# Optimization experiments

Hardware: AMD Instinct MI355X
Metric: run time of the kernel (lower is better)

Reference implementation:

```python
import jax, jax.numpy as jnp
import numpy as np

TEMPERATURE = 11.313708498984761  # sqrt(128)
TOP_K = 16
EPS = 10e-8


def sparse_attention(attn_s, top_k):
    # attn_s: [N, T]; keep top_k entries per row, shift by k-th value, clamp, renormalize
    T = attn_s.shape[1]
    if T <= top_k:
        return attn_s
    delta = jax.lax.top_k(attn_s, top_k)[0][:, -1] + EPS  # [N]
    w = jnp.maximum(attn_s - delta[:, None], 0.0)
    return w / (jnp.sum(w, axis=1, keepdims=True) + EPS)


def setup_inputs() -> dict:
    key = jax.random.key(0)
    kq, kk, kv = jax.random.split(key, 3)
    q = jax.random.normal(kq, (8, 4096, 128), dtype=jnp.float32)
    k = jax.random.normal(kk, (8, 4096, 128), dtype=jnp.float32)
    v = jax.random.normal(kv, (8, 1, 128), dtype=jnp.float32)
    return {"q": q, "k": k, "v": v}


def reference(q, k, v):
    # scores: [b, lq, lk]
    scores = jnp.einsum('bqd,bkd->bqk', q, k) / TEMPERATURE
    # max over keys (keepdim) then exp -> [b, lq, 1]
    scores = jnp.exp(jnp.max(scores, axis=-1, keepdims=True))
    b, lq, _ = scores.shape
    # flag=True: softmax over the query dimension (permute(0,2,1) then softmax(-1))
    attn = jax.nn.softmax(scores[:, :, 0], axis=-1)  # [b, lq]
    # Sparse_attention top-k over query dim (flag=True reshape path)
    sp = sparse_attention(attn, TOP_K)  # [b, lq]
    attn3 = sp[:, :, None]  # [b, lq, 1] (dropout p=0.0 -> identity)
    out = jnp.einsum('bqk,bkd->bqd', attn3, v)  # [b, lq, dv]
    extra_loss = 0.0
    return out, attn3, extra_loss
```

## Files before the change

### kernel.cpp

```cpp
#include <hip/hip_runtime.h>
#include <math.h>

typedef __attribute__((ext_vector_type(8)))  short short8v;
typedef __attribute__((ext_vector_type(4)))  short short4v;
typedef __attribute__((ext_vector_type(16))) float f32x16;

#define NB     8
#define SEQ    4096
#define DIM    128
#define KSPLIT 4
#define NSPAN  (SEQ / KSPLIT)
#define BN     64
#define BM     256
#define TEMP_INV (1.0f / 11.313708498984761f)
#define EPSF   1e-7f
#define NEGINF -3.0e38f

__device__ __forceinline__ unsigned short f2bf(float x) {
    unsigned u = __float_as_uint(x);
    return (unsigned short)((u + 0x7FFFu + ((u >> 16) & 1u)) >> 16);
}
__device__ __forceinline__ float bf2f(unsigned short h) {
    return __uint_as_float(((unsigned)h) << 16);
}
__device__ __forceinline__ unsigned umaxu(unsigned a, unsigned b) { return a > b ? a : b; }

#define GL_LDS16(gsrc, ldst)                                                              \
    __builtin_amdgcn_global_load_lds((const __attribute__((address_space(1))) void*)(gsrc), \
                                     (__attribute__((address_space(3))) void*)(ldst), 16, 0, 0)

__global__ __launch_bounds__(256) void split_khi_kernel(
    const float* __restrict__ kp, unsigned short* __restrict__ kh)
{
    int t    = blockIdx.x * 256 + threadIdx.x;
    int row  = t >> 2;
    int part = t & 3;
    const float* src = kp + (size_t)row * DIM + part * 32;
    unsigned short* dst = kh + (size_t)row * DIM;
    int key = (row & 15) << 3;
    #pragma unroll
    for (int c = 0; c < 4; ++c) {
        int d = part * 32 + c * 8;
        float4 x0 = *(const float4*)(src + c * 8);
        float4 x1 = *(const float4*)(src + c * 8 + 4);
        short8v h;
        h[0] = (short)f2bf(x0.x); h[1] = (short)f2bf(x0.y);
        h[2] = (short)f2bf(x0.z); h[3] = (short)f2bf(x0.w);
        h[4] = (short)f2bf(x1.x); h[5] = (short)f2bf(x1.y);
        h[6] = (short)f2bf(x1.z); h[7] = (short)f2bf(x1.w);
        *(short8v*)(dst + (d ^ key)) = h;
    }
}

__global__ __launch_bounds__(512, 4) void max_hi_kernel(
    const float* __restrict__ qp, const unsigned short* __restrict__ khp,
    unsigned int* __restrict__ cand)
{
    __shared__ __align__(16) unsigned short kbuf[2][BN * DIM];

    const int bid   = blockIdx.x;
    const int batch = bid & 7;
    const int qt    = (bid >> 3) & 15;
    const int ks    = bid >> 7;

    const int tid   = threadIdx.x;
    const int wv    = tid >> 6;
    const int lane  = tid & 63;
    const int lhalf = lane >> 5;
    const int l31   = lane & 31;
    const int qrow0 = qt * BM + wv * 32;

    const char* ktile0 = (const char*)(khp + ((size_t)(batch * SEQ + ks * NSPAN)) * DIM);
    const int   woff   = wv * 2048;

    #pragma unroll
    for (int r = 0; r < 2; ++r) {
        int off = woff + r * 1024;
        GL_LDS16(ktile0 + off + lane * 16, (char*)&kbuf[0][0] + off);
    }

    short8v ah[8];
    {
        const float* qrow = qp + ((size_t)(batch * SEQ + qrow0 + l31)) * DIM + lhalf * 8;
        #pragma unroll
        for (int ch = 0; ch < 8; ++ch) {
            float4 x0 = *(const float4*)(qrow + ch * 16);
            float4 x1 = *(const float4*)(qrow + ch * 16 + 4);
            short8v h;
            h[0] = (short)f2bf(x0.x); h[1] = (short)f2bf(x0.y);
            h[2] = (short)f2bf(x0.z); h[3] = (short)f2bf(x0.w);
            h[4] = (short)f2bf(x1.x); h[5] = (short)f2bf(x1.y);
            h[6] = (short)f2bf(x1.z); h[7] = (short)f2bf(x1.w);
            ah[ch] = h;
        }
    }

    unsigned pk0[16], pk1[16];
    #pragma unroll
    for (int r = 0; r < 16; ++r) { pk0[r] = 0u; pk1[r] = 0u; }

    __syncthreads();

    int cur = 0;
    for (int it = 0; it < NSPAN / BN; ++it) {
        if (it < NSPAN / BN - 1) {
            const char* src = ktile0 + (size_t)(it + 1) * (BN * 256);
            #pragma unroll
            for (int r = 0; r < 2; ++r) {
                int off = woff + r * 1024;
                GL_LDS16(src + off + lane * 16, (char*)&kbuf[cur ^ 1][0] + off);
            }
        }
        __builtin_amdgcn_s_setprio(1);
        const unsigned itb = (unsigned)it;
        #pragma unroll
        for (int ns = 0; ns < 2; ++ns) {
            const int  brow = ns * 32 + l31;
            const int  bkey = (l31 & 15) << 3;
            const char* base = (const char*)&kbuf[cur][0] + brow * 256;
            f32x16 c;
            #pragma unroll
            for (int r = 0; r < 16; ++r) c[r] = 0.f;
            #pragma unroll
            for (int ch = 0; ch < 8; ++ch) {
                const int boff = 2 * ((ch * 16 + lhalf * 8) ^ bkey);
                short8v bh = *(const short8v*)(base + boff);
                c = __builtin_amdgcn_mfma_f32_32x32x16_bf16(ah[ch], bh, c, 0, 0, 0);
            }
            #pragma unroll
            for (int r = 0; r < 16; ++r) {
                unsigned pv = (__float_as_uint(c[r] + 128.f) & 0xFFFFFFF0u) | itb;
                if (ns == 0) pk0[r] = umaxu(pk0[r], pv);
                else         pk1[r] = umaxu(pk1[r], pv);
            }
        }
        __builtin_amdgcn_s_setprio(0);
        __syncthreads();
        cur ^= 1;
    }

    #pragma unroll
    for (int r = 0; r < 16; ++r) {
        unsigned k0 = pk0[r], k1v = pk1[r];
        unsigned i0  = ((k0 & 15u) << 6)  | l31;
        unsigned i1v = ((k1v & 15u) << 6) | 32u | l31;
        unsigned t1, t1i, t2, t2i;
        if (k0 >= k1v) { t1 = k0;  t1i = i0;  t2 = k1v; t2i = i1v; }
        else           { t1 = k1v; t1i = i1v; t2 = k0;  t2i = i0;  }
        #pragma unroll
        for (int off = 1; off <= 16; off <<= 1) {
            unsigned o1  = (unsigned)__shfl_xor((int)t1,  off, 64);
            unsigned o1i = (unsigned)__shfl_xor((int)t1i, off, 64);
            unsigned o2  = (unsigned)__shfl_xor((int)t2,  off, 64);
            unsigned o2i = (unsigned)__shfl_xor((int)t2i, off, 64);
            bool og = o1 > t1;
            unsigned n1  = og ? o1  : t1;
            unsigned n1i = og ? o1i : t1i;
            unsigned a2  = og ? t1  : o1;
            unsigned a2i = og ? t1i : o1i;
            unsigned b2  = og ? o2  : t2;
            unsigned b2i = og ? o2i : t2i;
            bool ag = a2 > b2;
            t1 = n1; t1i = n1i;
            t2 = ag ? a2 : b2; t2i = ag ? a2i : b2i;
        }
        if (l31 == 0) {
            int rr = (r & 3) + 8 * (r >> 2) + 4 * lhalf;
            cand[((size_t)(batch * SEQ + qrow0 + rr)) * KSPLIT + ks] =
                (t1i & 0xFFFFu) | (t2i << 16);
        }
    }
}

__global__ __launch_bounds__(256) void rescore_kernel(
    const float* __restrict__ qp, const float* __restrict__ kp,
    const unsigned int* __restrict__ cand, float* __restrict__ mq)
{
    const int row  = blockIdx.x * 4 + (threadIdx.x >> 6);
    const int lane = threadIdx.x & 63;
    const int b    = row >> 12;
    const int g    = lane >> 3;
    const int t8   = lane & 7;
    const int ks   = g >> 1;
    unsigned cc  = cand[(size_t)row * KSPLIT + ks];
    unsigned idx = (g & 1) ? (cc >> 16) : (cc & 0xFFFFu);
    const float* qrow = qp + (size_t)row * DIM + t8 * 16;
    const float* krow = kp + ((size_t)(b * SEQ + ks * NSPAN + (int)idx)) * DIM + t8 * 16;
    float s = 0.f;
    #pragma unroll
    for (int i = 0; i < 4; ++i) {
        float4 a  = *(const float4*)(qrow + i * 4);
        float4 kk = *(const float4*)(krow + i * 4);
        s += a.x * kk.x + a.y * kk.y + a.z * kk.z + a.w * kk.w;
    }
    #pragma unroll
    for (int off = 1; off <= 4; off <<= 1) s += __shfl_xor(s, off, 64);
    #pragma unroll
    for (int off = 8; off <= 32; off <<= 1) s = fmaxf(s, __shfl_xor(s, off, 64));
    if (lane == 0) mq[row] = s * TEMP_INV;
}

__global__ __launch_bounds__(512, 2) void max_scores_kernel(
    const float* __restrict__ qp, const float* __restrict__ kp,
    float* __restrict__ mpart)
{
    __shared__ short khi[BN * DIM];
    __shared__ short klo[BN * DIM];

    const int bid   = blockIdx.x;
    const int batch = bid & 7;
    const int qt    = (bid >> 3) & 15;
    const int ks    = bid >> 7;
    const int tid   = threadIdx.x;
    const int wv    = tid >> 6;
    const int lane  = tid & 63;
    const int lhalf = lane >> 5;
    const int l31   = lane & 31;
    const int qrow0 = qt * BM + wv * 32;

    short8v ah[8], al[8];
    {
        const float* qrow = qp + ((size_t)(batch * SEQ + qrow0 + l31)) * DIM + lhalf * 8;
        #pragma unroll
        for (int ch = 0; ch < 8; ++ch) {
            float4 x0 = *(const float4*)(qrow + ch * 16);
            float4 x1 = *(const float4*)(qrow + ch * 16 + 4);
            float xs[8] = {x0.x, x0.y, x0.z, x0.w, x1.x, x1.y, x1.z, x1.w};
            short8v h, l;
            #pragma unroll
            for (int j = 0; j < 8; ++j) {
                unsigned short hb = f2bf(xs[j]);
                h[j] = (short)hb;
                l[j] = (short)f2bf(xs[j] - bf2f(hb));
            }
            ah[ch] = h; al[ch] = l;
        }
    }

    f32x16 mx;
    #pragma unroll
    for (int r = 0; r < 16; ++r) mx[r] = NEGINF;

    const int srow = tid >> 3;
    const int soct = tid & 7;
    const int skey = (srow & 15) << 3;

    for (int it = 0; it < NSPAN / BN; ++it) {
        const int n0 = ks * NSPAN + it * BN;
        __syncthreads();
        {
            const float* ksrc = kp + ((size_t)(batch * SEQ + n0 + srow)) * DIM + soct * 16;
            #pragma unroll
            for (int i = 0; i < 4; ++i) {
                float4 x = *(const float4*)(ksrc + i * 4);
                int dq  = soct * 16 + i * 4;
                int idx = srow * DIM + (dq ^ skey);
                float xs[4] = {x.x, x.y, x.z, x.w};
                short4v h, l;
                #pragma unroll
                for (int j = 0; j < 4; ++j) {
                    unsigned short hb = f2bf(xs[j]);
                    h[j] = (short)hb;
                    l[j] = (short)f2bf(xs[j] - bf2f(hb));
                }
                *(short4v*)(&khi[idx]) = h;
                *(short4v*)(&klo[idx]) = l;
            }
        }
        __syncthreads();

        #pragma unroll
        for (int ns = 0; ns < 2; ++ns) {
            const int brow = ns * 32 + l31;
            const int bkey = (brow & 15) << 3;
            f32x16 c;
            #pragma unroll
            for (int r = 0; r < 16; ++r) c[r] = 0.f;
            #pragma unroll
            for (int ch = 0; ch < 8; ++ch) {
                const int d0  = ch * 16 + lhalf * 8;
                const int idx = brow * DIM + (d0 ^ bkey);
                short8v bh = *(const short8v*)(&khi[idx]);
                short8v bl = *(const short8v*)(&klo[idx]);
                c = __builtin_amdgcn_mfma_f32_32x32x16_bf16(ah[ch], bh, c, 0, 0, 0);
                c = __builtin_amdgcn_mfma_f32_32x32x16_bf16(al[ch], bh, c, 0, 0, 0);
                c = __builtin_amdgcn_mfma_f32_32x32x16_bf16(ah[ch], bl, c, 0, 0, 0);
            }
            #pragma unroll
            for (int r = 0; r < 16; ++r) mx[r] = fmaxf(mx[r], c[r]);
        }
    }

    #pragma unroll
    for (int r = 0; r < 16; ++r) {
        float v = mx[r];
        #pragma unroll
        for (int off = 16; off; off >>= 1)
            v = fmaxf(v, __shfl_xor(v, off, 64));
        mx[r] = v;
    }
    if (l31 == 0) {
        #pragma unroll
        for (int r = 0; r < 16; ++r) {
            int rr = (r & 3) + 8 * (r >> 2) + 4 * lhalf;
            mpart[((size_t)(batch * SEQ + qrow0 + rr)) * KSPLIT + ks] = mx[r] * TEMP_INV;
        }
    }
}

__global__ void reduce4_kernel(const float* __restrict__ mpart, float* __restrict__ mq)
{
    int i = blockIdx.x * 256 + threadIdx.x;
    float4 mp = *(const float4*)(mpart + (size_t)i * 4);
    mq[i] = fmaxf(fmaxf(mp.x, mp.y), fmaxf(mp.z, mp.w));
}

__global__ __launch_bounds__(1024) void softmax_topk2_kernel(
    const float* __restrict__ mq, float* __restrict__ attn_out,
    float* __restrict__ loss_out)
{
    const int b    = blockIdx.x;
    const int tid  = threadIdx.x;
    const int wv   = tid >> 6;
    const int lane = tid & 63;
    __shared__ float cand[256];
    __shared__ float smZ[16], smW[16];
    __shared__ float bc[2];

    float m[4];
    #pragma unroll
    for (int j = 0; j < 4; ++j) m[j] = mq[b * SEQ + tid + j * 1024];

    {
        float a0 = m[0], a1 = m[1], a2 = m[2], a3 = m[3];
        for (int pass = 0; pass < 16; ++pass) {
            float v = fmaxf(fmaxf(a0, a1), fmaxf(a2, a3));
            #pragma unroll
            for (int off = 32; off; off >>= 1) v = fmaxf(v, __shfl_xor(v, off, 64));
            bool has = (a0 == v) || (a1 == v) || (a2 == v) || (a3 == v);
            unsigned long long msk = __ballot(has);
            int leader = __ffsll(msk) - 1;
            if (lane == leader) {
                if (a0 == v) a0 = NEGINF;
                else if (a1 == v) a1 = NEGINF;
                else if (a2 == v) a2 = NEGINF;
                else a3 = NEGINF;
            }
            if (lane == pass) cand[wv * 16 + pass] = v;
        }
    }
    __syncthreads();

    if (wv == 0) {
        float a0 = cand[lane * 4 + 0], a1 = cand[lane * 4 + 1];
        float a2 = cand[lane * 4 + 2], a3 = cand[lane * 4 + 3];
        float first = 0.f, last = 0.f;
        for (int pass = 0; pass < 16; ++pass) {
            float v = fmaxf(fmaxf(a0, a1), fmaxf(a2, a3));
            #pragma unroll
            for (int off = 32; off; off >>= 1) v = fmaxf(v, __shfl_xor(v, off, 64));
            bool has = (a0 == v) || (a1 == v) || (a2 == v) || (a3 == v);
            unsigned long long msk = __ballot(has);
            int leader = __ffsll(msk) - 1;
            if (lane == leader) {
                if (a0 == v) a0 = NEGINF;
                else if (a1 == v) a1 = NEGINF;
                else if (a2 == v) a2 = NEGINF;
                else a3 = NEGINF;
            }
            if (pass == 0) first = v;
            last = v;
        }
        if (lane == 0) { bc[0] = first; bc[1] = last; }
    }
    __syncthreads();

    const float S   = expf(bc[0]);
    const float m16 = bc[1];

    float e[4]; float ls = 0.f;
    #pragma unroll
    for (int j = 0; j < 4; ++j) { e[j] = expf(expf(m[j]) - S); ls += e[j]; }
    #pragma unroll
    for (int off = 32; off; off >>= 1) ls += __shfl_xor(ls, off, 64);
    if (lane == 0) smZ[wv] = ls;
    __syncthreads();
    float Z = 0.f;
    #pragma unroll
    for (int i = 0; i < 16; ++i) Z += smZ[i];

    const float a16   = expf(expf(m16) - S) / Z;
    const float delta = a16 + EPSF;

    float w0[4]; float lw = 0.f;
    #pragma unroll
    for (int j = 0; j < 4; ++j) { w0[j] = fmaxf(e[j] / Z - delta, 0.f); lw += w0[j]; }
    #pragma unroll
    for (int off = 32; off; off >>= 1) lw += __shfl_xor(lw, off, 64);
    if (lane == 0) smW[wv] = lw;
    __syncthreads();
    float W = 0.f;
    #pragma unroll
    for (int i = 0; i < 16; ++i) W += smW[i];
    const float rW = 1.f / (W + EPSF);

    #pragma unroll
    for (int j = 0; j < 4; ++j)
        attn_out[b * SEQ + tid + j * 1024] = w0[j] * rW;
    if (b == 0 && tid == 0) loss_out[0] = 0.f;
}

__global__ void broadcast_out_kernel(const float* __restrict__ sp,
                                     const float* __restrict__ vp,
                                     float* __restrict__ outp)
{
    int gid = blockIdx.x * 256 + threadIdx.x;
    int row = gid >> 5;
    int c4  = gid & 31;
    float  s  = sp[row];
    float4 vv = *(const float4*)(vp + (row >> 12) * DIM + c4 * 4);
    float4 o; o.x = s * vv.x; o.y = s * vv.y; o.z = s * vv.z; o.w = s * vv.w;
    *(float4*)(outp + (size_t)gid * 4) = o;
}

extern "C" void kernel_launch(void* const* d_in, const int* in_sizes, int n_in,
                              void* d_out, int out_size, void* d_ws, size_t ws_size,
                              hipStream_t stream)
{
    (void)in_sizes; (void)n_in; (void)out_size;
    const float* q = (const float*)d_in[0];
    const float* k = (const float*)d_in[1];
    const float* v = (const float*)d_in[2];
    float* out  = (float*)d_out;
    float* attn = out + (size_t)NB * SEQ * DIM;
    float* loss = attn + (size_t)NB * SEQ;

    const size_t KH_BYTES   = (size_t)NB * SEQ * DIM * 2;
    const size_t CAND_BYTES = (size_t)NB * SEQ * KSPLIT * 4;
    const size_t MQ_BYTES   = (size_t)NB * SEQ * 4;

    if (ws_size >= KH_BYTES + CAND_BYTES + MQ_BYTES) {
        unsigned short* kh  = (unsigned short*)d_ws;
        unsigned int* cand  = (unsigned int*)((char*)d_ws + KH_BYTES);
        float* mq           = (float*)((char*)d_ws + KH_BYTES + CAND_BYTES);
        hipLaunchKernelGGL(split_khi_kernel, dim3(NB * SEQ * 4 / 256), dim3(256), 0, stream, k, kh);
        hipLaunchKernelGGL(max_hi_kernel, dim3(NB * (SEQ / BM) * KSPLIT), dim3(512), 0, stream,
                           q, kh, cand);
        hipLaunchKernelGGL(rescore_kernel, dim3(NB * SEQ / 4), dim3(256), 0, stream,
                           q, k, cand, mq);
        hipLaunchKernelGGL(softmax_topk2_kernel, dim3(NB), dim3(1024), 0, stream, mq, attn, loss);
    } else {
        float* mpart = (float*)d_ws;
        float* mq    = mpart + (size_t)NB * SEQ * KSPLIT;
        hipLaunchKernelGGL(max_scores_kernel, dim3(NB * (SEQ / BM) * KSPLIT), dim3(512), 0, stream,
                           q, k, mpart);
        hipLaunchKernelGGL(reduce4_kernel, dim3(NB * SEQ / 256), dim3(256), 0, stream, mpart, mq);
        hipLaunchKernelGGL(softmax_topk2_kernel, dim3(NB), dim3(1024), 0, stream, mq, attn, loss);
    }
    hipLaunchKernelGGL(broadcast_out_kernel, dim3((NB * SEQ * DIM / 4) / 256), dim3(256), 0, stream,
                       attn, v, out);
}
```

Baseline: 166.3 us.

## Enlarge max-score tiles so each wave computes two query blocks per K fragment

The bf16 max-score kernel now uses 512-row query tiles and 128-key K tiles. Each wave holds two 32-row query fragments and reuses every LDS K fragment for two MFMA chains, which halves LDS reads per MFMA and halves the grid. The +128 bias is folded into the initial accumulator, and the packed key/index now uses a 5-bit field. The candidate tracking changes from top-2 per lane over two column blocks to top-1 per lane, then a top-2 shuffle reduction. The cost is higher register pressure (occupancy hint lowered to 2), double the LDS per block, and fewer mantissa bits kept in the packed max.

```diff
diff --git a/kernel.cpp b/kernel.cpp
--- a/kernel.cpp
+++ b/kernel.cpp
@@ -12,6 +12,9 @@
 #define NSPAN  (SEQ / KSPLIT)
 #define BN     64
 #define BM     256
+#define BN2    128
+#define BM2    512
+#define ITERS  (NSPAN / BN2)
 #define TEMP_INV (1.0f / 11.313708498984761f)
 #define EPSF   1e-7f
 #define NEGINF -3.0e38f
@@ -52,36 +55,37 @@
     }
 }
 
-__global__ __launch_bounds__(512, 4) void max_hi_kernel(
+__global__ __launch_bounds__(512, 2) void max_hi2_kernel(
     const float* __restrict__ qp, const unsigned short* __restrict__ khp,
     unsigned int* __restrict__ cand)
 {
-    __shared__ __align__(16) unsigned short kbuf[2][BN * DIM];
+    __shared__ __align__(16) unsigned short kbuf[2][BN2 * DIM];
 
     const int bid   = blockIdx.x;
     const int batch = bid & 7;
-    const int qt    = (bid >> 3) & 15;
-    const int ks    = bid >> 7;
+    const int qt    = (bid >> 3) & 7;
+    const int ks    = bid >> 6;
 
     const int tid   = threadIdx.x;
     const int wv    = tid >> 6;
     const int lane  = tid & 63;
     const int lhalf = lane >> 5;
     const int l31   = lane & 31;
-    const int qrow0 = qt * BM + wv * 32;
+    const int qrow0 = qt * BM2 + wv * 64;
 
     const char* ktile0 = (const char*)(khp + ((size_t)(batch * SEQ + ks * NSPAN)) * DIM);
-    const int   woff   = wv * 2048;
-
-    #pragma unroll
-    for (int r = 0; r < 2; ++r) {
+    const int   woff   = wv * 4096;
+
+    #pragma unroll
+    for (int r = 0; r < 4; ++r) {
         int off = woff + r * 1024;
         GL_LDS16(ktile0 + off + lane * 16, (char*)&kbuf[0][0] + off);
     }
 
-    short8v ah[8];
-    {
-        const float* qrow = qp + ((size_t)(batch * SEQ + qrow0 + l31)) * DIM + lhalf * 8;
+    short8v ah[2][8];
+    #pragma unroll
+    for (int s = 0; s < 2; ++s) {
+        const float* qrow = qp + ((size_t)(batch * SEQ + qrow0 + s * 32 + l31)) * DIM + lhalf * 8;
         #pragma unroll
         for (int ch = 0; ch < 8; ++ch) {
             float4 x0 = *(const float4*)(qrow + ch * 16);
@@ -91,9 +95,13 @@
             h[2] = (short)f2bf(x0.z); h[3] = (short)f2bf(x0.w);
             h[4] = (short)f2bf(x1.x); h[5] = (short)f2bf(x1.y);
             h[6] = (short)f2bf(x1.z); h[7] = (short)f2bf(x1.w);
-            ah[ch] = h;
-        }
-    }
+            ah[s][ch] = h;
+        }
+    }
+
+    f32x16 c128;
+    #pragma unroll
+    for (int r = 0; r < 16; ++r) c128[r] = 128.f;
 
     unsigned pk0[16], pk1[16];
     #pragma unroll
@@ -102,36 +110,37 @@
     __syncthreads();
 
     int cur = 0;
-    for (int it = 0; it < NSPAN / BN; ++it) {
-        if (it < NSPAN / BN - 1) {
-            const char* src = ktile0 + (size_t)(it + 1) * (BN * 256);
-            #pragma unroll
-            for (int r = 0; r < 2; ++r) {
+    for (int it = 0; it < ITERS; ++it) {
+        if (it < ITERS - 1) {
+            const char* src = ktile0 + (size_t)(it + 1) * (BN2 * 256);
+            #pragma unroll
+            for (int r = 0; r < 4; ++r) {
                 int off = woff + r * 1024;
                 GL_LDS16(src + off + lane * 16, (char*)&kbuf[cur ^ 1][0] + off);
             }
         }
         __builtin_amdgcn_s_setprio(1);
-        const unsigned itb = (unsigned)it;
-        #pragma unroll
-        for (int ns = 0; ns < 2; ++ns) {
+        const unsigned itf = (unsigned)(it << 2);
+        #pragma unroll
+        for (int ns = 0; ns < 4; ++ns) {
             const int  brow = ns * 32 + l31;
             const int  bkey = (l31 & 15) << 3;
             const char* base = (const char*)&kbuf[cur][0] + brow * 256;
-            f32x16 c;
-            #pragma unroll
-            for (int r = 0; r < 16; ++r) c[r] = 0.f;
-            #pragma unroll
-            for (int ch = 0; ch < 8; ++ch) {
+            const unsigned fld = itf | (unsigned)ns;
+            short8v bh0 = *(const short8v*)(base + 2 * ((lhalf * 8) ^ bkey));
+            f32x16 c0 = __builtin_amdgcn_mfma_f32_32x32x16_bf16(ah[0][0], bh0, c128, 0, 0, 0);
+            f32x16 c1 = __builtin_amdgcn_mfma_f32_32x32x16_bf16(ah[1][0], bh0, c128, 0, 0, 0);
+            #pragma unroll
+            for (int ch = 1; ch < 8; ++ch) {
                 const int boff = 2 * ((ch * 16 + lhalf * 8) ^ bkey);
                 short8v bh = *(const short8v*)(base + boff);
-                c = __builtin_amdgcn_mfma_f32_32x32x16_bf16(ah[ch], bh, c, 0, 0, 0);
+                c0 = __builtin_amdgcn_mfma_f32_32x32x16_bf16(ah[0][ch], bh, c0, 0, 0, 0);
+                c1 = __builtin_amdgcn_mfma_f32_32x32x16_bf16(ah[1][ch], bh, c1, 0, 0, 0);
             }
             #pragma unroll
             for (int r = 0; r < 16; ++r) {
-                unsigned pv = (__float_as_uint(c[r] + 128.f) & 0xFFFFFFF0u) | itb;
-                if (ns == 0) pk0[r] = umaxu(pk0[r], pv);
-                else         pk1[r] = umaxu(pk1[r], pv);
+                pk0[r] = umaxu(pk0[r], (__float_as_uint(c0[r]) & 0xFFFFFFE0u) | fld);
+                pk1[r] = umaxu(pk1[r], (__float_as_uint(c1[r]) & 0xFFFFFFE0u) | fld);
             }
         }
         __builtin_amdgcn_s_setprio(0);
@@ -140,34 +149,36 @@
     }
 
     #pragma unroll
-    for (int r = 0; r < 16; ++r) {
-        unsigned k0 = pk0[r], k1v = pk1[r];
-        unsigned i0  = ((k0 & 15u) << 6)  | l31;
-        unsigned i1v = ((k1v & 15u) << 6) | 32u | l31;
-        unsigned t1, t1i, t2, t2i;
-        if (k0 >= k1v) { t1 = k0;  t1i = i0;  t2 = k1v; t2i = i1v; }
-        else           { t1 = k1v; t1i = i1v; t2 = k0;  t2i = i0;  }
-        #pragma unroll
-        for (int off = 1; off <= 16; off <<= 1) {
-            unsigned o1  = (unsigned)__shfl_xor((int)t1,  off, 64);
-            unsigned o1i = (unsigned)__shfl_xor((int)t1i, off, 64);
-            unsigned o2  = (unsigned)__shfl_xor((int)t2,  off, 64);
-            unsigned o2i = (unsigned)__shfl_xor((int)t2i, off, 64);
-            bool og = o1 > t1;
-            unsigned n1  = og ? o1  : t1;
-            unsigned n1i = og ? o1i : t1i;
-            unsigned a2  = og ? t1  : o1;
-            unsigned a2i = og ? t1i : o1i;
-            unsigned b2  = og ? o2  : t2;
-            unsigned b2i = og ? o2i : t2i;
-            bool ag = a2 > b2;
-            t1 = n1; t1i = n1i;
-            t2 = ag ? a2 : b2; t2i = ag ? a2i : b2i;
-        }
-        if (l31 == 0) {
-            int rr = (r & 3) + 8 * (r >> 2) + 4 * lhalf;
-            cand[((size_t)(batch * SEQ + qrow0 + rr)) * KSPLIT + ks] =
-                (t1i & 0xFFFFu) | (t2i << 16);
+    for (int s = 0; s < 2; ++s) {
+        #pragma unroll
+        for (int r = 0; r < 16; ++r) {
+            unsigned key = (s == 0) ? pk0[r] : pk1[r];
+            unsigned f   = key & 31u;
+            unsigned t1  = key;
+            unsigned t1i = (f >> 2) * 128u + (f & 3u) * 32u + (unsigned)l31;
+            unsigned t2  = 0u, t2i = 0u;
+            #pragma unroll
+            for (int off = 1; off <= 16; off <<= 1) {
+                unsigned o1  = (unsigned)__shfl_xor((int)t1,  off, 64);
+                unsigned o1i = (unsigned)__shfl_xor((int)t1i, off, 64);
+                unsigned o2  = (unsigned)__shfl_xor((int)t2,  off, 64);
+                unsigned o2i = (unsigned)__shfl_xor((int)t2i, off, 64);
+                bool og = o1 > t1;
+                unsigned n1  = og ? o1  : t1;
+                unsigned n1i = og ? o1i : t1i;
+                unsigned a2  = og ? t1  : o1;
+                unsigned a2i = og ? t1i : o1i;
+                unsigned b2  = og ? o2  : t2;
+                unsigned b2i = og ? o2i : t2i;
+                bool ag = a2 > b2;
+                t1 = n1; t1i = n1i;
+                t2 = ag ? a2 : b2; t2i = ag ? a2i : b2i;
+            }
+            if (l31 == 0) {
+                int rr = (r & 3) + 8 * (r >> 2) + 4 * lhalf;
+                cand[((size_t)(batch * SEQ + qrow0 + s * 32 + rr)) * KSPLIT + ks] =
+                    (t1i & 0xFFFFu) | (t2i << 16);
+            }
         }
     }
 }
@@ -444,7 +455,7 @@
         unsigned int* cand  = (unsigned int*)((char*)d_ws + KH_BYTES);
         float* mq           = (float*)((char*)d_ws + KH_BYTES + CAND_BYTES);
         hipLaunchKernelGGL(split_khi_kernel, dim3(NB * SEQ * 4 / 256), dim3(256), 0, stream, k, kh);
-        hipLaunchKernelGGL(max_hi_kernel, dim3(NB * (SEQ / BM) * KSPLIT), dim3(512), 0, stream,
+        hipLaunchKernelGGL(max_hi2_kernel, dim3(NB * (SEQ / BM2) * KSPLIT), dim3(512), 0, stream,
                            q, kh, cand);
         hipLaunchKernelGGL(rescore_kernel, dim3(NB * SEQ / 4), dim3(256), 0, stream,
                            q, k, cand, mq);
```

Result: no change. 163.3 us (-1.8%).
